# Kernel optimization log

Hardware: AMD Instinct MI355X
Metric: run time of the kernel (lower is better)

## Reference

```python
import jax, jax.numpy as jnp
import numpy as np

N_G, N_D = 100000, 50000
E_GG, E_DG = 1600000, 800000
IN, HID, H, OUT = 128, 128, 8, 2
D = HID // H  # 16


def setup_inputs() -> dict:
    key = jax.random.key(0)
    ks = jax.random.split(key, 14)
    w = lambda k, s: jax.random.normal(k, s, dtype=jnp.float32) * 0.05
    return {
        "x_gene": jax.random.normal(ks[0], (N_G, IN), dtype=jnp.float32),
        "x_disease": jax.random.normal(ks[1], (N_D, IN), dtype=jnp.float32),
        "edge_gg": jax.random.randint(ks[2], (2, E_GG), 0, N_G),   # gene -> gene
        "edge_dg": jax.random.randint(ks[3], (2, E_DG), 0, N_D),   # disease -> gene (dst < N_D <= N_G)
        "proj_gene_w": w(ks[4], (HID, IN)),
        "proj_gene_b": jnp.zeros((HID,), jnp.float32),
        "proj_disease_w": w(ks[5], (HID, IN)),
        "proj_disease_b": jnp.zeros((HID,), jnp.float32),
        "att_src_gg": w(ks[6], (H, D)),
        "att_dst_gg": w(ks[7], (H, D)),
        "att_src_dg": w(ks[8], (H, D)),
        "att_dst_dg": w(ks[9], (H, D)),
        "k_lin_w": w(ks[10], (HID, HID)),
        "k_lin_b": jnp.zeros((HID,), jnp.float32),
        "q": w(ks[11], (HID,)),
        "lin_w": w(ks[12], (OUT, HID)),
        "lin_b": jnp.zeros((OUT,), jnp.float32),
    }


def _edge_type_out(x_src, x_dst, att_src, att_dst, src, dst, num_dst):
    """GAT-style message passing for one edge type. x_*: [N,H,D]."""
    a_s = (x_src * att_src).sum(-1)          # [Ns, H]
    a_d = (x_dst * att_dst).sum(-1)          # [Nd, H]
    a = a_s[src] + a_d[dst]                  # [E, H]
    a = jnp.where(a > 0, a, 0.2 * a)         # leaky_relu(0.2)
    # segment softmax over edges grouped by dst node
    m = jax.ops.segment_max(a, dst, num_segments=num_dst)
    m = jnp.where(jnp.isfinite(m), m, 0.0)
    e = jnp.exp(a - m[dst])
    s = jax.ops.segment_sum(e, dst, num_segments=num_dst)
    alpha = e / (s[dst] + 1e-16)             # [E, H]
    msg = x_src[src] * alpha[:, :, None]     # [E, H, D]
    out = jax.ops.segment_sum(msg, dst, num_segments=num_dst)
    return jax.nn.relu(out.reshape(num_dst, H * D))


def reference(x_gene, x_disease, edge_gg, edge_dg,
              proj_gene_w, proj_gene_b, proj_disease_w, proj_disease_b,
              att_src_gg, att_dst_gg, att_src_dg, att_dst_dg,
              k_lin_w, k_lin_b, q, lin_w, lin_b):
    # per-node-type projection, split into heads
    xg = (x_gene @ proj_gene_w.T + proj_gene_b).reshape(N_G, H, D)
    xd = (x_disease @ proj_disease_w.T + proj_disease_b).reshape(N_D, H, D)

    # node-level attention per edge type (dropout p=0.6 is train-only; eval mode here)
    out_gg = _edge_type_out(xg, xg, att_src_gg, att_dst_gg, edge_gg[0], edge_gg[1], N_G)
    out_dg = _edge_type_out(xd, xg, att_src_dg, att_dst_dg, edge_dg[0], edge_dg[1], N_G)

    # semantic-level attention across metapaths for dst type 'gene'
    outs = jnp.stack([out_gg, out_dg])                  # [2, N_G, HID]
    k = jnp.tanh(outs @ k_lin_w.T + k_lin_b)            # [2, N_G, HID]
    score = (q * k.mean(axis=1)).sum(-1)                # [2]
    attn = jax.nn.softmax(score, axis=0)
    fused = (attn[:, None, None] * outs).sum(0)         # [N_G, HID]

    return fused @ lin_w.T + lin_b                      # [N_G, OUT]
```

## Files before the change

### kernel.cpp

```cpp
#include <hip/hip_runtime.h>
#include <hip/hip_fp16.h>
#include <math.h>

#define NG 100000
#define ND 50000
#define EGG 1600000
#define EDG 800000
#define EALL (EGG + EDG)
#define NALL (NG + NG)
#define HID 128
#define NH 8

#define SHIFT 10
#define BDSTS (1 << SHIFT)
#define NBUK  ((NALL + BDSTS - 1) / BDSTS)
#define BUKCAP 18432
#define S1_CH 3072
#define KM_HALF ((NG + 127) / 128)

#define OFF_OUT_GG 0UL
#define OFF_OUT_DG 6400000UL
#define OFF_XG     12800000UL
#define OFF_XD     19200000UL
#define OFF_ASG    22400000UL
#define OFF_ADG    23200000UL
#define OFF_ADD    24000000UL
#define OFF_ASD    24800000UL
#define OFF_KPART  25200000UL
#define OFF_BCNT   25200256UL
#define ZERO_BASE  OFF_KPART
#define ZERO_CNT   512
#define OFF_ATTN   25200768UL
#define OFF_RP     25200896UL
#define OFF_COL    25400960UL
#define OFF_WTIL   27800960UL
#define OFF_BTIL   27804032UL
#define OFF_WTILD  27804160UL
#define OFF_BTILD  27805184UL

typedef float  f32x4  __attribute__((ext_vector_type(4)));
typedef short  bf16x8 __attribute__((ext_vector_type(8)));
typedef _Float16 f16x8 __attribute__((ext_vector_type(8)));
#define MFMA(a, b, c)  __builtin_amdgcn_mfma_f32_16x16x32_bf16(a, b, c, 0, 0, 0)
#define MFMAH(a, b, c) __builtin_amdgcn_mfma_f32_16x16x32_f16(a, b, c, 0, 0, 0)

#define FMAMIX_LO(ACC, SRC, AL) \
    asm("v_fma_mix_f32 %0, %1, %2, %0 op_sel:[0,0,0] op_sel_hi:[1,0,0]" \
        : "+v"(ACC) : "v"(SRC), "v"(AL))
#define FMAMIX_HI(ACC, SRC, AL) \
    asm("v_fma_mix_f32 %0, %1, %2, %0 op_sel:[1,0,0] op_sel_hi:[1,0,0]" \
        : "+v"(ACC) : "v"(SRC), "v"(AL))

__device__ __forceinline__ unsigned short bf16_rne(float f) {
    unsigned u = __float_as_uint(f);
    u += 0x7FFFu + ((u >> 16) & 1u);
    return (unsigned short)(u >> 16);
}
__device__ __forceinline__ float bf16f(unsigned short h) {
    return __uint_as_float(((unsigned)h) << 16);
}
__device__ __forceinline__ unsigned short f16_bits(float f) {
    __half h = __float2half(f);
    return *(unsigned short*)&h;
}
__device__ __forceinline__ float fast_tanh(float x) {
    x = fminf(fmaxf(x, -15.f), 15.f);
    float t = __expf(2.f * x);
    return (t - 1.f) / (t + 1.f);
}
__device__ __forceinline__ bf16x8 cvt_hi8(f32x4 v0, f32x4 v1) {
    bf16x8 f;
    f[0] = (short)bf16_rne(v0.x); f[1] = (short)bf16_rne(v0.y);
    f[2] = (short)bf16_rne(v0.z); f[3] = (short)bf16_rne(v0.w);
    f[4] = (short)bf16_rne(v1.x); f[5] = (short)bf16_rne(v1.y);
    f[6] = (short)bf16_rne(v1.z); f[7] = (short)bf16_rne(v1.w);
    return f;
}
__device__ __forceinline__ bf16x8 cvt_lo8(f32x4 v0, f32x4 v1, bf16x8 h) {
    bf16x8 f;
    f[0] = (short)bf16_rne(v0.x - bf16f((unsigned short)h[0]));
    f[1] = (short)bf16_rne(v0.y - bf16f((unsigned short)h[1]));
    f[2] = (short)bf16_rne(v0.z - bf16f((unsigned short)h[2]));
    f[3] = (short)bf16_rne(v0.w - bf16f((unsigned short)h[3]));
    f[4] = (short)bf16_rne(v1.x - bf16f((unsigned short)h[4]));
    f[5] = (short)bf16_rne(v1.y - bf16f((unsigned short)h[5]));
    f[6] = (short)bf16_rne(v1.z - bf16f((unsigned short)h[6]));
    f[7] = (short)bf16_rne(v1.w - bf16f((unsigned short)h[7]));
    return f;
}
__device__ __forceinline__ unsigned relu_pk(unsigned u) {
    return u & ~(((u & 0x80008000u) >> 15) * 0xFFFFu);
}
union U4F16 { uint4 u; f16x8 f; };

__global__ void init_zero_k(float* __restrict__ p, int n) {
    int i = blockIdx.x * 256 + threadIdx.x;
    if (i < n) p[i] = 0.f;
}

__device__ __forceinline__ void wtil_body(const float* __restrict__ W,
                                          const float* __restrict__ bias,
                                          const float* __restrict__ a0,
                                          const float* __restrict__ a1,
                                          const float* __restrict__ a2, int natt,
                                          float* __restrict__ wtil, float* __restrict__ btil,
                                          int bid, int nblk) {
    int tot = natt * 8 * 128;
    for (int i = bid * 256 + threadIdx.x; i < tot; i += nblk * 256) {
        int k = i & 127, cc = i >> 7;
        int v = cc >> 3, h = cc & 7;
        const float* av = (v == 0) ? a0 : (v == 1) ? a1 : a2;
        float s = 0.f;
        #pragma unroll
        for (int c = 0; c < 16; c++) s += av[h * 16 + c] * W[(h * 16 + c) * 128 + k];
        wtil[i] = s;
    }
    if (bid == 0 && threadIdx.x < natt * 8) {
        int v = threadIdx.x >> 3, h = threadIdx.x & 7;
        const float* av = (v == 0) ? a0 : (v == 1) ? a1 : a2;
        float s = 0.f;
        #pragma unroll
        for (int c = 0; c < 16; c++) s += av[h * 16 + c] * bias[h * 16 + c];
        btil[threadIdx.x] = s;
    }
}

__global__ void make_wtil_both(const float* __restrict__ Wg, const float* __restrict__ bg,
                               const float* __restrict__ ag0, const float* __restrict__ ag1,
                               const float* __restrict__ ag2,
                               const float* __restrict__ Wd, const float* __restrict__ bd,
                               const float* __restrict__ ad0,
                               float* __restrict__ wtilG, float* __restrict__ btilG,
                               float* __restrict__ wtilD, float* __restrict__ btilD) {
    if (blockIdx.x < 8)
        wtil_body(Wg, bg, ag0, ag1, ag2, 3, wtilG, btilG, blockIdx.x, 8);
    else
        wtil_body(Wd, bd, ad0, ad0, ad0, 1, wtilD, btilD, blockIdx.x - 8, 4);
}

template<int NATT>
__launch_bounds__(256)
__global__ void proj_mfma(const float* __restrict__ x, const float* __restrict__ W,
                          const float* __restrict__ bias,
                          const float* __restrict__ wtil, const float* __restrict__ btil,
                          unsigned short* __restrict__ xbf,
                          float* __restrict__ o0, float* __restrict__ o1,
                          float* __restrict__ o2, int N) {
    constexpr int NTE = (NATT * 8 + 15) / 16;
    constexpr int NT = 8 + NTE;
    __shared__ bf16x8 Bhi[NT * 4 * 64];
    __shared__ bf16x8 Blo[8 * 4 * 64];
    for (int idx = threadIdx.x; idx < 128 * 32; idx += 256) {
        int row = idx >> 5, kq = idx & 31;
        f32x4 v = *(const f32x4*)&W[row * 128 + kq * 4];
        int ct = row >> 4, c = row & 15;
        int k0 = kq * 4;
        int kc = k0 >> 5, q16 = (k0 & 31) >> 3, j2 = (k0 & 7) >> 1;
        int slot = (ct * 4 + kc) * 64 + q16 * 16 + c;
        unsigned short hx = bf16_rne(v.x), hy = bf16_rne(v.y);
        unsigned short hz = bf16_rne(v.z), hw = bf16_rne(v.w);
        unsigned* dh = (unsigned*)&Bhi[slot];
        dh[j2]     = ((unsigned)hy << 16) | hx;
        dh[j2 + 1] = ((unsigned)hw << 16) | hz;
        unsigned* dl = (unsigned*)&Blo[slot];
        dl[j2]     = ((unsigned)bf16_rne(v.y - bf16f(hy)) << 16) | bf16_rne(v.x - bf16f(hx));
        dl[j2 + 1] = ((unsigned)bf16_rne(v.w - bf16f(hw)) << 16) | bf16_rne(v.z - bf16f(hz));
    }
    for (int idx = threadIdx.x; idx < NTE * 16 * 32; idx += 256) {
        int cc = idx >> 5, kq = idx & 31;
        f32x4 v = {0.f, 0.f, 0.f, 0.f};
        if (cc < NATT * 8) v = *(const f32x4*)&wtil[cc * 128 + kq * 4];
        int ct = 8 + (cc >> 4), c = cc & 15;
        int k0 = kq * 4;
        int kc = k0 >> 5, q16 = (k0 & 31) >> 3, j2 = (k0 & 7) >> 1;
        unsigned* dh = (unsigned*)&Bhi[(ct * 4 + kc) * 64 + q16 * 16 + c];
        dh[j2]     = ((unsigned)bf16_rne(v.y) << 16) | bf16_rne(v.x);
        dh[j2 + 1] = ((unsigned)bf16_rne(v.w) << 16) | bf16_rne(v.z);
    }
    __syncthreads();
    int wv = threadIdx.x >> 6, l = threadIdx.x & 63;
    int q = l >> 4, c16 = l & 15;
    int rw = blockIdx.x * 128 + wv * 32;
    int n0 = min(rw + c16, N - 1);
    int n1 = min(rw + 16 + c16, N - 1);
    const float* xr0 = &x[(size_t)n0 * 128 + q * 8];
    const float* xr1 = &x[(size_t)n1 * 128 + q * 8];
    #define LOADX(FH, FL, PTR, OFF) \
        bf16x8 FH, FL; \
        { f32x4 v0_ = *(const f32x4*)((PTR) + (OFF)); \
          f32x4 v1_ = *(const f32x4*)((PTR) + (OFF) + 4); \
          FH = cvt_hi8(v0_, v1_); FL = cvt_lo8(v0_, v1_, FH); }
    LOADX(xh00, xl00, xr0, 0)  LOADX(xh01, xl01, xr0, 32)
    LOADX(xh02, xl02, xr0, 64) LOADX(xh03, xl03, xr0, 96)
    LOADX(xh10, xl10, xr1, 0)  LOADX(xh11, xl11, xr1, 32)
    LOADX(xh12, xl12, xr1, 64) LOADX(xh13, xl13, xr1, 96)
    #undef LOADX
    int r0 = rw + q * 4;
    int r1 = r0 + 16;
    #define CT_MAIN(CT) { \
        bf16x8 bh0 = Bhi[((CT) * 4 + 0) * 64 + l]; \
        bf16x8 bh1 = Bhi[((CT) * 4 + 1) * 64 + l]; \
        bf16x8 bh2 = Bhi[((CT) * 4 + 2) * 64 + l]; \
        bf16x8 bh3 = Bhi[((CT) * 4 + 3) * 64 + l]; \
        bf16x8 bl0 = Blo[((CT) * 4 + 0) * 64 + l]; \
        bf16x8 bl1 = Blo[((CT) * 4 + 1) * 64 + l]; \
        bf16x8 bl2 = Blo[((CT) * 4 + 2) * 64 + l]; \
        bf16x8 bl3 = Blo[((CT) * 4 + 3) * 64 + l]; \
        f32x4 aA = {0,0,0,0}, aB = {0,0,0,0}, aC = {0,0,0,0}, aD = {0,0,0,0}; \
        aA = MFMA(xh00, bh0, aA); aB = MFMA(xh01, bh1, aB); \
        aC = MFMA(xh10, bh0, aC); aD = MFMA(xh11, bh1, aD); \
        aA = MFMA(xl00, bh0, aA); aB = MFMA(xl01, bh1, aB); \
        aC = MFMA(xl10, bh0, aC); aD = MFMA(xl11, bh1, aD); \
        aA = MFMA(xh00, bl0, aA); aB = MFMA(xh01, bl1, aB); \
        aC = MFMA(xh10, bl0, aC); aD = MFMA(xh11, bl1, aD); \
        aA = MFMA(xh02, bh2, aA); aB = MFMA(xh03, bh3, aB); \
        aC = MFMA(xh12, bh2, aC); aD = MFMA(xh13, bh3, aD); \
        aA = MFMA(xl02, bh2, aA); aB = MFMA(xl03, bh3, aB); \
        aC = MFMA(xl12, bh2, aC); aD = MFMA(xl13, bh3, aD); \
        aA = MFMA(xh02, bl2, aA); aB = MFMA(xh03, bl3, aB); \
        aC = MFMA(xh12, bl2, aC); aD = MFMA(xh13, bl3, aD); \
        f32x4 d0 = aA + aB, d1 = aC + aD; \
        float bv = bias[(CT) * 16 + c16]; \
        int col = (CT) * 16 + c16; \
        if (r0 + 0 < N) xbf[(size_t)(r0 + 0) * 128 + col] = f16_bits(d0[0] + bv); \
        if (r0 + 1 < N) xbf[(size_t)(r0 + 1) * 128 + col] = f16_bits(d0[1] + bv); \
        if (r0 + 2 < N) xbf[(size_t)(r0 + 2) * 128 + col] = f16_bits(d0[2] + bv); \
        if (r0 + 3 < N) xbf[(size_t)(r0 + 3) * 128 + col] = f16_bits(d0[3] + bv); \
        if (r1 + 0 < N) xbf[(size_t)(r1 + 0) * 128 + col] = f16_bits(d1[0] + bv); \
        if (r1 + 1 < N) xbf[(size_t)(r1 + 1) * 128 + col] = f16_bits(d1[1] + bv); \
        if (r1 + 2 < N) xbf[(size_t)(r1 + 2) * 128 + col] = f16_bits(d1[2] + bv); \
        if (r1 + 3 < N) xbf[(size_t)(r1 + 3) * 128 + col] = f16_bits(d1[3] + bv); }
    CT_MAIN(0) CT_MAIN(1) CT_MAIN(2) CT_MAIN(3)
    CT_MAIN(4) CT_MAIN(5) CT_MAIN(6) CT_MAIN(7)
    #undef CT_MAIN
    #define CT_ATT(TE) { \
        bf16x8 bh0 = Bhi[((8 + (TE)) * 4 + 0) * 64 + l]; \
        bf16x8 bh1 = Bhi[((8 + (TE)) * 4 + 1) * 64 + l]; \
        bf16x8 bh2 = Bhi[((8 + (TE)) * 4 + 2) * 64 + l]; \
        bf16x8 bh3 = Bhi[((8 + (TE)) * 4 + 3) * 64 + l]; \
        f32x4 aA = {0,0,0,0}, aB = {0,0,0,0}, aC = {0,0,0,0}, aD = {0,0,0,0}; \
        aA = MFMA(xh00, bh0, aA); aB = MFMA(xh01, bh1, aB); \
        aC = MFMA(xh10, bh0, aC); aD = MFMA(xh11, bh1, aD); \
        aA = MFMA(xh02, bh2, aA); aB = MFMA(xh03, bh3, aB); \
        aC = MFMA(xh12, bh2, aC); aD = MFMA(xh13, bh3, aD); \
        f32x4 d0 = aA + aB, d1 = aC + aD; \
        int cc = (TE) * 16 + c16; \
        if (cc < NATT * 8) { \
            float bt = btil[cc]; \
            int v = cc >> 3, h = cc & 7; \
            float* op = (v == 0) ? o0 : ((v == 1) ? o1 : o2); \
            if (r0 + 0 < N) op[(r0 + 0) * 8 + h] = d0[0] + bt; \
            if (r0 + 1 < N) op[(r0 + 1) * 8 + h] = d0[1] + bt; \
            if (r0 + 2 < N) op[(r0 + 2) * 8 + h] = d0[2] + bt; \
            if (r0 + 3 < N) op[(r0 + 3) * 8 + h] = d0[3] + bt; \
            if (r1 + 0 < N) op[(r1 + 0) * 8 + h] = d1[0] + bt; \
            if (r1 + 1 < N) op[(r1 + 1) * 8 + h] = d1[1] + bt; \
            if (r1 + 2 < N) op[(r1 + 2) * 8 + h] = d1[2] + bt; \
            if (r1 + 3 < N) op[(r1 + 3) * 8 + h] = d1[3] + bt; } }
    CT_ATT(0)
    if constexpr (NTE > 1) { CT_ATT(1) }
    #undef CT_ATT
}

__launch_bounds__(256)
__global__ void fused_scatter(const int* __restrict__ gg_src, const int* __restrict__ gg_dst,
                              const int* __restrict__ dg_src, const int* __restrict__ dg_dst,
                              int* __restrict__ bcnt, unsigned int* __restrict__ colPacked) {
    __shared__ int cnt[256], scanE[256], gbase[256], cursor[256];
    __shared__ int ss[256];
    __shared__ unsigned int sorted[S1_CH];
    __shared__ unsigned char bof[S1_CH];
    int t = threadIdx.x;
    cnt[t] = 0;
    __syncthreads();
    int base = blockIdx.x * S1_CH;
    for (int k = 0; k < S1_CH; k += 256) {
        int e = base + k + t;
        if (e < EALL) {
            int dn = (e < EGG) ? gg_dst[e] : (NG + dg_dst[e - EGG]);
            atomicAdd(&cnt[dn >> SHIFT], 1);
        }
    }
    __syncthreads();
    int v = cnt[t];
    ss[t] = v;
    __syncthreads();
    for (int off = 1; off < 256; off <<= 1) {
        int y = (t >= off) ? ss[t - off] : 0;
        __syncthreads();
        ss[t] += y;
        __syncthreads();
    }
    scanE[t] = ss[t] - v;
    cursor[t] = ss[t] - v;
    if (t < NBUK && v > 0) gbase[t] = atomicAdd(&bcnt[t], v);
    __syncthreads();
    for (int k = 0; k < S1_CH; k += 256) {
        int e = base + k + t;
        if (e < EALL) {
            int s, dn;
            if (e < EGG) { s = gg_src[e]; dn = gg_dst[e]; }
            else         { s = dg_src[e - EGG]; dn = NG + dg_dst[e - EGG]; }
            int b = dn >> SHIFT;
            int slot = atomicAdd(&cursor[b], 1);
            sorted[slot] = ((unsigned int)s << SHIFT) | (unsigned int)(dn & (BDSTS - 1));
            bof[slot] = (unsigned char)b;
        }
    }
    __syncthreads();
    int total = ss[255];
    for (int f = t; f < total; f += 256) {
        int b = bof[f];
        colPacked[(size_t)b * BUKCAP + gbase[b] + (f - scanE[b])] = sorted[f];
    }
}

__launch_bounds__(256)
__global__ void bucket_build(const unsigned int* __restrict__ colPacked,
                             const int* __restrict__ bcnt,
                             int* __restrict__ rp, int* __restrict__ col) {
    __shared__ int lcur[BDSTS];
    __shared__ int tsum[256];
    __shared__ int bscan[256];
    int b = blockIdx.x;
    int t = threadIdx.x;
    bscan[t] = (t < NBUK) ? bcnt[t] : 0;
    __syncthreads();
    for (int off = 1; off < 256; off <<= 1) {
        int y = (t >= off) ? bscan[t - off] : 0;
        __syncthreads();
        bscan[t] += y;
        __syncthreads();
    }
    int gb = (b > 0) ? bscan[b - 1] : 0;
    int d0 = b << SHIFT;
    int nd = min(BDSTS, NALL - d0);
    int cnt = bcnt[b];
    const unsigned int* pk = colPacked + (size_t)b * BUKCAP;
    for (int i = t; i < BDSTS; i += 256) lcur[i] = 0;
    __syncthreads();
    for (int i = t; i < cnt; i += 256)
        atomicAdd(&lcur[pk[i] & (BDSTS - 1)], 1);
    __syncthreads();
    int h0 = lcur[t * 4 + 0], h1 = lcur[t * 4 + 1], h2 = lcur[t * 4 + 2], h3 = lcur[t * 4 + 3];
    int tot = h0 + h1 + h2 + h3;
    tsum[t] = tot;
    __syncthreads();
    for (int off = 1; off < 256; off <<= 1) {
        int y = (t >= off) ? tsum[t - off] : 0;
        __syncthreads();
        tsum[t] += y;
        __syncthreads();
    }
    int pp = tsum[t] - tot + gb;
    __syncthreads();
    #define EMIT(J, HJ) { int idx = t * 4 + (J); \
        if (idx < nd) rp[d0 + idx] = pp; \
        lcur[idx] = pp; pp += (HJ); }
    EMIT(0, h0) EMIT(1, h1) EMIT(2, h2) EMIT(3, h3)
    #undef EMIT
    if (b == NBUK - 1 && t == 0) rp[NALL] = EALL;
    __syncthreads();
    for (int i = t; i < cnt; i += 256) {
        unsigned int p = pk[i];
        int pos = atomicAdd(&lcur[p & (BDSTS - 1)], 1);
        col[pos] = (int)(p >> SHIFT);
    }
}

__launch_bounds__(256)
__global__ void gat_gather_all(const int* __restrict__ rp, const int* __restrict__ col,
                               const float* __restrict__ as_gg, const float* __restrict__ ad_gg,
                               const unsigned short* __restrict__ xg_h,
                               const float* __restrict__ as_dg, const float* __restrict__ ad_dg,
                               const unsigned short* __restrict__ xd_h,
                               unsigned short* __restrict__ out_gg,
                               unsigned short* __restrict__ out_dg) {
    int wid = (blockIdx.x * 256 + threadIdx.x) >> 6;
    int l = threadIdx.x & 63;
    if (wid >= NALL) return;
    int isdg = wid >= NG;
    int d = isdg ? wid - NG : wid;
    const float* a_s = isdg ? as_dg : as_gg;
    const float* a_d = isdg ? ad_dg : ad_gg;
    const unsigned short* xbf = isdg ? xd_h : xg_h;
    unsigned short* outh = (isdg ? out_dg : out_gg);

    int base = rp[wid];
    int deg = rp[wid + 1] - base;

    int hl = l & 7;
    int g  = l >> 3;
    float adl = a_d[d * 8 + hl];
    int q = l >> 4;
    int cq = l & 15;
    int hq = cq >> 1;
    uint32_t colbyte = (uint32_t)cq << 4;
    float a0 = 0.f, a1 = 0.f, a2 = 0.f, a3 = 0.f, a4 = 0.f, a5 = 0.f, a6 = 0.f, a7 = 0.f;
    float sacc = 0.f;
    for (int c0 = 0; c0 < deg; c0 += 64) {
        int myi = c0 + l;
        int colreg = (myi < deg) ? col[base + myi] : 0;
        int lim = min(deg - c0, 64);
        for (int j8 = 0; j8 < lim; j8 += 8) {
            float ex;
            {
                int s = __shfl(colreg, j8 + g);
                float a = a_s[s * 8 + hl] + adl;
                a = a > 0.f ? a : 0.2f * a;
                ex = __expf(a);
            }
            int jlim = min(lim - j8, 8);
            #pragma unroll
            for (int sub = 0; sub < 8; sub += 4) {
                int jrel = sub + q;
                int s = __shfl(colreg, j8 + jrel);
                float al = __shfl(ex, (jrel << 3) + hq);
                al = (jrel < jlim) ? al : 0.f;
                sacc += al;
                const uint4 rv = *(const uint4*)((const char*)xbf +
                                    (((size_t)(uint32_t)s << 8) + colbyte));
                FMAMIX_LO(a0, rv.x, al); FMAMIX_HI(a1, rv.x, al);
                FMAMIX_LO(a2, rv.y, al); FMAMIX_HI(a3, rv.y, al);
                FMAMIX_LO(a4, rv.z, al); FMAMIX_HI(a5, rv.z, al);
                FMAMIX_LO(a6, rv.w, al); FMAMIX_HI(a7, rv.w, al);
            }
        }
    }
    sacc += __shfl_xor(sacc, 16); sacc += __shfl_xor(sacc, 32);
    a0 += __shfl_xor(a0, 16); a0 += __shfl_xor(a0, 32);
    a1 += __shfl_xor(a1, 16); a1 += __shfl_xor(a1, 32);
    a2 += __shfl_xor(a2, 16); a2 += __shfl_xor(a2, 32);
    a3 += __shfl_xor(a3, 16); a3 += __shfl_xor(a3, 32);
    a4 += __shfl_xor(a4, 16); a4 += __shfl_xor(a4, 32);
    a5 += __shfl_xor(a5, 16); a5 += __shfl_xor(a5, 32);
    a6 += __shfl_xor(a6, 16); a6 += __shfl_xor(a6, 32);
    a7 += __shfl_xor(a7, 16); a7 += __shfl_xor(a7, 32);
    if (q == 0) {
        float rsc = 1.f / (sacc + 1e-16f);
        a0 *= rsc; a1 *= rsc; a2 *= rsc; a3 *= rsc;
        a4 *= rsc; a5 *= rsc; a6 *= rsc; a7 *= rsc;
        __half2 h01 = __floats2half2_rn(a0, a1);
        __half2 h23 = __floats2half2_rn(a2, a3);
        __half2 h45 = __floats2half2_rn(a4, a5);
        __half2 h67 = __floats2half2_rn(a6, a7);
        uint4 o;
        o.x = *(unsigned*)&h01; o.y = *(unsigned*)&h23;
        o.z = *(unsigned*)&h45; o.w = *(unsigned*)&h67;
        *(uint4*)((char*)outh + (size_t)d * 256 + cq * 16) = o;
    }
}

__launch_bounds__(256)
__global__ void kmean_mfma(const unsigned short* __restrict__ srcA,
                           const unsigned short* __restrict__ srcB,
                           const float* __restrict__ W, const float* __restrict__ bias,
                           float* __restrict__ kp) {
    __shared__ f16x8 Bs[8 * 4 * 64];
    for (int idx = threadIdx.x; idx < 128 * 32; idx += 256) {
        int row = idx >> 5, kq = idx & 31;
        f32x4 v = *(const f32x4*)&W[row * 128 + kq * 4];
        int ct = row >> 4, c = row & 15;
        int k0 = kq * 4;
        int kc = k0 >> 5, q16 = (k0 & 31) >> 3, j2 = (k0 & 7) >> 1;
        unsigned* dst = (unsigned*)&Bs[(ct * 4 + kc) * 64 + q16 * 16 + c];
        dst[j2]     = ((unsigned)f16_bits(v.y) << 16) | f16_bits(v.x);
        dst[j2 + 1] = ((unsigned)f16_bits(v.w) << 16) | f16_bits(v.z);
    }
    __syncthreads();
    int half = blockIdx.x >= KM_HALF;
    const unsigned short* src = half ? srcB : srcA;
    float* kpp = half ? (kp + 128) : kp;
    int rb = (half ? blockIdx.x - KM_HALF : blockIdx.x) * 128;
    int wv = threadIdx.x >> 6, l = threadIdx.x & 63;
    int q = l >> 4, c16 = l & 15;
    int rw = rb + wv * 32;
    const char* xr0 = (const char*)src + (size_t)(rw + c16) * 256 + q * 16;
    const char* xr1 = xr0 + 16 * 256;
    #define LOADA(F, PTR, OFF) f16x8 F; { \
        U4F16 u_; u_.u = *(const uint4*)((PTR) + (OFF)); \
        u_.u.x = relu_pk(u_.u.x); u_.u.y = relu_pk(u_.u.y); \
        u_.u.z = relu_pk(u_.u.z); u_.u.w = relu_pk(u_.u.w); \
        F = u_.f; }
    LOADA(f00, xr0, 0) LOADA(f01, xr0, 64) LOADA(f02, xr0, 128) LOADA(f03, xr0, 192)
    LOADA(f10, xr1, 0) LOADA(f11, xr1, 64) LOADA(f12, xr1, 128) LOADA(f13, xr1, 192)
    #undef LOADA
    float bv0 = bias[c16],      bv1 = bias[16 + c16], bv2 = bias[32 + c16], bv3 = bias[48 + c16];
    float bv4 = bias[64 + c16], bv5 = bias[80 + c16], bv6 = bias[96 + c16], bv7 = bias[112 + c16];
    int row0 = rw + q * 4;
    int row1 = row0 + 16;
    float cs0 = 0.f, cs1 = 0.f, cs2 = 0.f, cs3 = 0.f, cs4 = 0.f, cs5 = 0.f, cs6 = 0.f, cs7 = 0.f;
    #define CT_STEP(CT, CS, BV) { \
        f16x8 b0 = Bs[((CT) * 4 + 0) * 64 + l]; \
        f16x8 b1 = Bs[((CT) * 4 + 1) * 64 + l]; \
        f16x8 b2 = Bs[((CT) * 4 + 2) * 64 + l]; \
        f16x8 b3 = Bs[((CT) * 4 + 3) * 64 + l]; \
        f32x4 aA = {0,0,0,0}, aB = {0,0,0,0}, aC = {0,0,0,0}, aD = {0,0,0,0}; \
        aA = MFMAH(f00, b0, aA); aB = MFMAH(f01, b1, aB); \
        aA = MFMAH(f02, b2, aA); aB = MFMAH(f03, b3, aB); \
        aC = MFMAH(f10, b0, aC); aD = MFMAH(f11, b1, aD); \
        aC = MFMAH(f12, b2, aC); aD = MFMAH(f13, b3, aD); \
        f32x4 d0 = aA + aB, d1 = aC + aD; \
        float s = 0.f; \
        if (row0 + 0 < NG) s += fast_tanh(d0[0] + (BV)); \
        if (row0 + 1 < NG) s += fast_tanh(d0[1] + (BV)); \
        if (row0 + 2 < NG) s += fast_tanh(d0[2] + (BV)); \
        if (row0 + 3 < NG) s += fast_tanh(d0[3] + (BV)); \
        if (row1 + 0 < NG) s += fast_tanh(d1[0] + (BV)); \
        if (row1 + 1 < NG) s += fast_tanh(d1[1] + (BV)); \
        if (row1 + 2 < NG) s += fast_tanh(d1[2] + (BV)); \
        if (row1 + 3 < NG) s += fast_tanh(d1[3] + (BV)); \
        CS += s; }
    CT_STEP(0, cs0, bv0) CT_STEP(1, cs1, bv1) CT_STEP(2, cs2, bv2) CT_STEP(3, cs3, bv3)
    CT_STEP(4, cs4, bv4) CT_STEP(5, cs5, bv5) CT_STEP(6, cs6, bv6) CT_STEP(7, cs7, bv7)
    #undef CT_STEP
    __syncthreads();
    float* red = (float*)Bs;
    #define REDUCE_CT(CT, CS) { \
        float v = (CS); \
        v += __shfl_xor(v, 16); v += __shfl_xor(v, 32); \
        if (l < 16) red[wv * 128 + (CT) * 16 + l] = v; }
    REDUCE_CT(0, cs0) REDUCE_CT(1, cs1) REDUCE_CT(2, cs2) REDUCE_CT(3, cs3)
    REDUCE_CT(4, cs4) REDUCE_CT(5, cs5) REDUCE_CT(6, cs6) REDUCE_CT(7, cs7)
    #undef REDUCE_CT
    __syncthreads();
    if (threadIdx.x < 128) {
        float s = red[threadIdx.x] + red[128 + threadIdx.x]
                + red[256 + threadIdx.x] + red[384 + threadIdx.x];
        atomicAdd(&kpp[threadIdx.x], s);
    }
}

__global__ void score_attn(const float* __restrict__ kpart, const float* __restrict__ q,
                           float* __restrict__ attn) {
    __shared__ float r0[128], r1[128];
    int t = threadIdx.x;
    r0[t] = q[t] * kpart[t];
    r1[t] = q[t] * kpart[128 + t];
    __syncthreads();
    for (int s = 64; s > 0; s >>= 1) {
        if (t < s) { r0[t] += r0[t + s]; r1[t] += r1[t + s]; }
        __syncthreads();
    }
    if (t == 0) {
        float s0 = r0[0] / (float)NG, s1 = r1[0] / (float)NG;
        float mx = fmaxf(s0, s1);
        float e0 = expf(s0 - mx), e1 = expf(s1 - mx);
        attn[0] = e0 / (e0 + e1);
        attn[1] = e1 / (e0 + e1);
    }
}

__launch_bounds__(256)
__global__ void final_lin(const unsigned short* __restrict__ gg,
                          const unsigned short* __restrict__ dgb,
                          const float* __restrict__ attn, const float* __restrict__ lin_w,
                          const float* __restrict__ lin_b, float* __restrict__ outp) {
    int wid = (blockIdx.x * 256 + threadIdx.x) >> 6;
    int l = threadIdx.x & 63;
    if (wid >= NG) return;
    float a0 = attn[0], a1 = attn[1];
    unsigned gu = *(const unsigned*)((const char*)gg + (size_t)wid * 256 + l * 4);
    unsigned du = *(const unsigned*)((const char*)dgb + (size_t)wid * 256 + l * 4);
    float2 gv = __half22float2(*(const __half2*)&gu);
    float2 dv = __half22float2(*(const __half2*)&du);
    float fx = a0 * fmaxf(gv.x, 0.f) + a1 * fmaxf(dv.x, 0.f);
    float fy = a0 * fmaxf(gv.y, 0.f) + a1 * fmaxf(dv.y, 0.f);
    float2 w0 = *(const float2*)&lin_w[l * 2];
    float2 w1 = *(const float2*)&lin_w[128 + l * 2];
    float p0 = fx * w0.x + fy * w0.y;
    float p1 = fx * w1.x + fy * w1.y;
    for (int off = 32; off > 0; off >>= 1) {
        p0 += __shfl_down(p0, off);
        p1 += __shfl_down(p1, off);
    }
    if (l == 0) {
        float2 o;
        o.x = p0 + lin_b[0];
        o.y = p1 + lin_b[1];
        *(float2*)&outp[wid * 2] = o;
    }
}

extern "C" void kernel_launch(void* const* d_in, const int* in_sizes, int n_in,
                              void* d_out, int out_size, void* d_ws, size_t ws_size,
                              hipStream_t stream) {
    const float* x_gene    = (const float*)d_in[0];
    const float* x_disease = (const float*)d_in[1];
    const int*   edge_gg   = (const int*)d_in[2];
    const int*   edge_dg   = (const int*)d_in[3];
    const float* pg_w      = (const float*)d_in[4];
    const float* pg_b      = (const float*)d_in[5];
    const float* pd_w      = (const float*)d_in[6];
    const float* pd_b      = (const float*)d_in[7];
    const float* att_src_gg= (const float*)d_in[8];
    const float* att_dst_gg= (const float*)d_in[9];
    const float* att_src_dg= (const float*)d_in[10];
    const float* att_dst_dg= (const float*)d_in[11];
    const float* k_lin_w   = (const float*)d_in[12];
    const float* k_lin_b   = (const float*)d_in[13];
    const float* q         = (const float*)d_in[14];
    const float* lin_w     = (const float*)d_in[15];
    const float* lin_b     = (const float*)d_in[16];
    float* out = (float*)d_out;
    float* ws  = (float*)d_ws;

    unsigned short* out_gg = (unsigned short*)(ws + OFF_OUT_GG);
    unsigned short* out_dg = (unsigned short*)(ws + OFF_OUT_DG);
    unsigned int* colPacked = (unsigned int*)(ws + OFF_OUT_GG);
    unsigned short* xg_h = (unsigned short*)(ws + OFF_XG);
    unsigned short* xd_h = (unsigned short*)(ws + OFF_XD);
    float* a_src_gg = ws + OFF_ASG;
    float* a_dst_gg = ws + OFF_ADG;
    float* a_dst_dg = ws + OFF_ADD;
    float* a_src_dg = ws + OFF_ASD;
    float* kpart  = ws + OFF_KPART;
    float* attn   = ws + OFF_ATTN;
    float* wtilG  = ws + OFF_WTIL;
    float* btilG  = ws + OFF_BTIL;
    float* wtilD  = ws + OFF_WTILD;
    float* btilD  = ws + OFF_BTILD;
    int* bcnt  = (int*)(ws + OFF_BCNT);
    int* rp    = (int*)(ws + OFF_RP);
    int* col   = (int*)(ws + OFF_COL);

    const int* gg_src = edge_gg;
    const int* gg_dst = edge_gg + EGG;
    const int* dg_src = edge_dg;
    const int* dg_dst = edge_dg + EDG;

    hipLaunchKernelGGL(init_zero_k, dim3(2), dim3(256), 0, stream, ws + ZERO_BASE, ZERO_CNT);
    hipLaunchKernelGGL(make_wtil_both, dim3(12), dim3(256), 0, stream,
                       pg_w, pg_b, att_src_gg, att_dst_gg, att_dst_dg,
                       pd_w, pd_b, att_src_dg, wtilG, btilG, wtilD, btilD);
    hipLaunchKernelGGL((proj_mfma<3>), dim3((NG + 127) / 128), dim3(256), 0, stream,
                       x_gene, pg_w, pg_b, wtilG, btilG, xg_h,
                       a_src_gg, a_dst_gg, a_dst_dg, NG);
    hipLaunchKernelGGL((proj_mfma<1>), dim3((ND + 127) / 128), dim3(256), 0, stream,
                       x_disease, pd_w, pd_b, wtilD, btilD, xd_h,
                       a_src_dg, (float*)nullptr, (float*)nullptr, ND);
    hipLaunchKernelGGL(fused_scatter, dim3((EALL + S1_CH - 1) / S1_CH), dim3(256), 0, stream,
                       gg_src, gg_dst, dg_src, dg_dst, bcnt, colPacked);
    hipLaunchKernelGGL(bucket_build, dim3(NBUK), dim3(256), 0, stream,
                       colPacked, bcnt, rp, col);
    hipLaunchKernelGGL(gat_gather_all, dim3((NALL + 3) / 4), dim3(256), 0, stream,
                       rp, col, a_src_gg, a_dst_gg, xg_h, a_src_dg, a_dst_dg, xd_h,
                       out_gg, out_dg);
    hipLaunchKernelGGL(kmean_mfma, dim3(KM_HALF * 2), dim3(256), 0, stream,
                       out_gg, out_dg, k_lin_w, k_lin_b, kpart);
    hipLaunchKernelGGL(score_attn, dim3(1), dim3(128), 0, stream, kpart, q, attn);
    hipLaunchKernelGGL(final_lin, dim3((NG + 3) / 4), dim3(256), 0, stream,
                       out_gg, out_dg, attn, lin_w, lin_b, out);
}
```

Baseline: 327.1 us.

## Merge projection kernels and fold final linear projection into gather

Drops the separate wtil kernel. Each projection block now computes its attention-folded weights and biases in shared memory, and the gene and disease projections run as one launch. The final linear layer is applied per metapath inside the gather kernel, which writes 2-wide partial outputs, so the last kernel only mixes them with the attention weights instead of re-reading both 128-wide fp16 outputs. The gather does a little more work per node, and every projection block repeats the wtil computation.

```diff
diff --git a/kernel.cpp b/kernel.cpp
--- a/kernel.cpp
+++ b/kernel.cpp
@@ -17,6 +17,8 @@
 #define BUKCAP 18432
 #define S1_CH 3072
 #define KM_HALF ((NG + 127) / 128)
+#define GBLK ((NG + 127) / 128)
+#define DBLK ((ND + 127) / 128)
 
 #define OFF_OUT_GG 0UL
 #define OFF_OUT_DG 6400000UL
@@ -33,10 +35,8 @@
 #define OFF_ATTN   25200768UL
 #define OFF_RP     25200896UL
 #define OFF_COL    25400960UL
-#define OFF_WTIL   27800960UL
-#define OFF_BTIL   27804032UL
-#define OFF_WTILD  27804160UL
-#define OFF_BTILD  27805184UL
+#define OFF_PGG    27801088UL
+#define OFF_PDG    28001088UL
 
 typedef float  f32x4  __attribute__((ext_vector_type(4)));
 typedef short  bf16x8 __attribute__((ext_vector_type(8)));
@@ -98,58 +98,35 @@
     if (i < n) p[i] = 0.f;
 }
 
-__device__ __forceinline__ void wtil_body(const float* __restrict__ W,
-                                          const float* __restrict__ bias,
-                                          const float* __restrict__ a0,
-                                          const float* __restrict__ a1,
-                                          const float* __restrict__ a2, int natt,
-                                          float* __restrict__ wtil, float* __restrict__ btil,
-                                          int bid, int nblk) {
-    int tot = natt * 8 * 128;
-    for (int i = bid * 256 + threadIdx.x; i < tot; i += nblk * 256) {
-        int k = i & 127, cc = i >> 7;
-        int v = cc >> 3, h = cc & 7;
-        const float* av = (v == 0) ? a0 : (v == 1) ? a1 : a2;
-        float s = 0.f;
-        #pragma unroll
-        for (int c = 0; c < 16; c++) s += av[h * 16 + c] * W[(h * 16 + c) * 128 + k];
-        wtil[i] = s;
-    }
-    if (bid == 0 && threadIdx.x < natt * 8) {
-        int v = threadIdx.x >> 3, h = threadIdx.x & 7;
-        const float* av = (v == 0) ? a0 : (v == 1) ? a1 : a2;
-        float s = 0.f;
-        #pragma unroll
-        for (int c = 0; c < 16; c++) s += av[h * 16 + c] * bias[h * 16 + c];
-        btil[threadIdx.x] = s;
-    }
-}
-
-__global__ void make_wtil_both(const float* __restrict__ Wg, const float* __restrict__ bg,
-                               const float* __restrict__ ag0, const float* __restrict__ ag1,
-                               const float* __restrict__ ag2,
-                               const float* __restrict__ Wd, const float* __restrict__ bd,
-                               const float* __restrict__ ad0,
-                               float* __restrict__ wtilG, float* __restrict__ btilG,
-                               float* __restrict__ wtilD, float* __restrict__ btilD) {
-    if (blockIdx.x < 8)
-        wtil_body(Wg, bg, ag0, ag1, ag2, 3, wtilG, btilG, blockIdx.x, 8);
-    else
-        wtil_body(Wd, bd, ad0, ad0, ad0, 1, wtilD, btilD, blockIdx.x - 8, 4);
-}
-
-template<int NATT>
 __launch_bounds__(256)
-__global__ void proj_mfma(const float* __restrict__ x, const float* __restrict__ W,
-                          const float* __restrict__ bias,
-                          const float* __restrict__ wtil, const float* __restrict__ btil,
-                          unsigned short* __restrict__ xbf,
-                          float* __restrict__ o0, float* __restrict__ o1,
-                          float* __restrict__ o2, int N) {
-    constexpr int NTE = (NATT * 8 + 15) / 16;
-    constexpr int NT = 8 + NTE;
-    __shared__ bf16x8 Bhi[NT * 4 * 64];
+__global__ void proj_both(const float* __restrict__ xg, const float* __restrict__ Wg,
+                          const float* __restrict__ bg,
+                          const float* __restrict__ ag0, const float* __restrict__ ag1,
+                          const float* __restrict__ ag2,
+                          unsigned short* __restrict__ xgh,
+                          float* __restrict__ og0, float* __restrict__ og1,
+                          float* __restrict__ og2,
+                          const float* __restrict__ xd, const float* __restrict__ Wd,
+                          const float* __restrict__ bd, const float* __restrict__ ad0,
+                          unsigned short* __restrict__ xdh, float* __restrict__ od0) {
+    __shared__ bf16x8 Bhi[10 * 4 * 64];
     __shared__ bf16x8 Blo[8 * 4 * 64];
+    __shared__ float btilS[32];
+    int gene = blockIdx.x < GBLK;
+    const float* x    = gene ? xg : xd;
+    const float* W    = gene ? Wg : Wd;
+    const float* bias = gene ? bg : bd;
+    const float* a0v  = gene ? ag0 : ad0;
+    const float* a1v  = gene ? ag1 : ad0;
+    const float* a2v  = gene ? ag2 : ad0;
+    unsigned short* xbf = gene ? xgh : xdh;
+    float* o0 = gene ? og0 : od0;
+    float* o1 = og1;
+    float* o2 = og2;
+    int ccmax = gene ? 24 : 8;
+    int N = gene ? NG : ND;
+    int bid = gene ? blockIdx.x : blockIdx.x - GBLK;
+
     for (int idx = threadIdx.x; idx < 128 * 32; idx += 256) {
         int row = idx >> 5, kq = idx & 31;
         f32x4 v = *(const f32x4*)&W[row * 128 + kq * 4];
@@ -166,10 +143,19 @@
         dl[j2]     = ((unsigned)bf16_rne(v.y - bf16f(hy)) << 16) | bf16_rne(v.x - bf16f(hx));
         dl[j2 + 1] = ((unsigned)bf16_rne(v.w - bf16f(hw)) << 16) | bf16_rne(v.z - bf16f(hz));
     }
-    for (int idx = threadIdx.x; idx < NTE * 16 * 32; idx += 256) {
+    for (int idx = threadIdx.x; idx < 2 * 16 * 32; idx += 256) {
         int cc = idx >> 5, kq = idx & 31;
         f32x4 v = {0.f, 0.f, 0.f, 0.f};
-        if (cc < NATT * 8) v = *(const f32x4*)&wtil[cc * 128 + kq * 4];
+        if (cc < ccmax) {
+            int vv = cc >> 3, h = cc & 7;
+            const float* av = (vv == 0) ? a0v : (vv == 1) ? a1v : a2v;
+            #pragma unroll
+            for (int c = 0; c < 16; c++) {
+                float a = av[h * 16 + c];
+                f32x4 w = *(const f32x4*)&W[(h * 16 + c) * 128 + kq * 4];
+                v.x += a * w.x; v.y += a * w.y; v.z += a * w.z; v.w += a * w.w;
+            }
+        }
         int ct = 8 + (cc >> 4), c = cc & 15;
         int k0 = kq * 4;
         int kc = k0 >> 5, q16 = (k0 & 31) >> 3, j2 = (k0 & 7) >> 1;
@@ -177,10 +163,20 @@
         dh[j2]     = ((unsigned)bf16_rne(v.y) << 16) | bf16_rne(v.x);
         dh[j2 + 1] = ((unsigned)bf16_rne(v.w) << 16) | bf16_rne(v.z);
     }
+    if (threadIdx.x < 32) {
+        float s = 0.f;
+        if (threadIdx.x < ccmax) {
+            int vv = threadIdx.x >> 3, h = threadIdx.x & 7;
+            const float* av = (vv == 0) ? a0v : (vv == 1) ? a1v : a2v;
+            #pragma unroll
+            for (int c = 0; c < 16; c++) s += av[h * 16 + c] * bias[h * 16 + c];
+        }
+        btilS[threadIdx.x] = s;
+    }
     __syncthreads();
     int wv = threadIdx.x >> 6, l = threadIdx.x & 63;
     int q = l >> 4, c16 = l & 15;
-    int rw = blockIdx.x * 128 + wv * 32;
+    int rw = bid * 128 + wv * 32;
     int n0 = min(rw + c16, N - 1);
     int n1 = min(rw + 16 + c16, N - 1);
     const float* xr0 = &x[(size_t)n0 * 128 + q * 8];
@@ -245,10 +241,10 @@
         aC = MFMA(xh12, bh2, aC); aD = MFMA(xh13, bh3, aD); \
         f32x4 d0 = aA + aB, d1 = aC + aD; \
         int cc = (TE) * 16 + c16; \
-        if (cc < NATT * 8) { \
-            float bt = btil[cc]; \
-            int v = cc >> 3, h = cc & 7; \
-            float* op = (v == 0) ? o0 : ((v == 1) ? o1 : o2); \
+        if (cc < ccmax) { \
+            float bt = btilS[cc]; \
+            int vv = cc >> 3, h = cc & 7; \
+            float* op = (vv == 0) ? o0 : ((vv == 1) ? o1 : o2); \
             if (r0 + 0 < N) op[(r0 + 0) * 8 + h] = d0[0] + bt; \
             if (r0 + 1 < N) op[(r0 + 1) * 8 + h] = d0[1] + bt; \
             if (r0 + 2 < N) op[(r0 + 2) * 8 + h] = d0[2] + bt; \
@@ -258,7 +254,7 @@
             if (r1 + 2 < N) op[(r1 + 2) * 8 + h] = d1[2] + bt; \
             if (r1 + 3 < N) op[(r1 + 3) * 8 + h] = d1[3] + bt; } }
     CT_ATT(0)
-    if constexpr (NTE > 1) { CT_ATT(1) }
+    if (ccmax > 16) { CT_ATT(1) }
     #undef CT_ATT
 }
 
@@ -375,7 +371,9 @@
                                const float* __restrict__ as_dg, const float* __restrict__ ad_dg,
                                const unsigned short* __restrict__ xd_h,
                                unsigned short* __restrict__ out_gg,
-                               unsigned short* __restrict__ out_dg) {
+                               unsigned short* __restrict__ out_dg,
+                               const float* __restrict__ lin_w,
+                               float* __restrict__ pgg, float* __restrict__ pdg) {
     int wid = (blockIdx.x * 256 + threadIdx.x) >> 6;
     int l = threadIdx.x & 63;
     if (wid >= NALL) return;
@@ -448,6 +446,25 @@
         o.x = *(unsigned*)&h01; o.y = *(unsigned*)&h23;
         o.z = *(unsigned*)&h45; o.w = *(unsigned*)&h67;
         *(uint4*)((char*)outh + (size_t)d * 256 + cq * 16) = o;
+        float r0 = fmaxf(a0, 0.f), r1 = fmaxf(a1, 0.f), r2 = fmaxf(a2, 0.f), r3 = fmaxf(a3, 0.f);
+        float r4 = fmaxf(a4, 0.f), r5 = fmaxf(a5, 0.f), r6 = fmaxf(a6, 0.f), r7 = fmaxf(a7, 0.f);
+        f32x4 w0a = *(const f32x4*)&lin_w[cq * 8];
+        f32x4 w0b = *(const f32x4*)&lin_w[cq * 8 + 4];
+        f32x4 w1a = *(const f32x4*)&lin_w[128 + cq * 8];
+        f32x4 w1b = *(const f32x4*)&lin_w[128 + cq * 8 + 4];
+        float p0 = r0 * w0a.x + r1 * w0a.y + r2 * w0a.z + r3 * w0a.w
+                 + r4 * w0b.x + r5 * w0b.y + r6 * w0b.z + r7 * w0b.w;
+        float p1 = r0 * w1a.x + r1 * w1a.y + r2 * w1a.z + r3 * w1a.w
+                 + r4 * w1b.x + r5 * w1b.y + r6 * w1b.z + r7 * w1b.w;
+        p0 += __shfl_xor(p0, 1); p1 += __shfl_xor(p1, 1);
+        p0 += __shfl_xor(p0, 2); p1 += __shfl_xor(p1, 2);
+        p0 += __shfl_xor(p0, 4); p1 += __shfl_xor(p1, 4);
+        p0 += __shfl_xor(p0, 8); p1 += __shfl_xor(p1, 8);
+        if (l == 0) {
+            float* pp = isdg ? pdg : pgg;
+            float2 pv; pv.x = p0; pv.y = p1;
+            *(float2*)&pp[d * 2] = pv;
+        }
     }
 }
 
@@ -551,35 +568,18 @@
     }
 }
 
-__launch_bounds__(256)
-__global__ void final_lin(const unsigned short* __restrict__ gg,
-                          const unsigned short* __restrict__ dgb,
-                          const float* __restrict__ attn, const float* __restrict__ lin_w,
-                          const float* __restrict__ lin_b, float* __restrict__ outp) {
-    int wid = (blockIdx.x * 256 + threadIdx.x) >> 6;
-    int l = threadIdx.x & 63;
-    if (wid >= NG) return;
+__global__ void final_combine(const float* __restrict__ pgg, const float* __restrict__ pdg,
+                              const float* __restrict__ attn, const float* __restrict__ lin_b,
+                              float* __restrict__ outp) {
+    int n = blockIdx.x * 256 + threadIdx.x;
+    if (n >= NG) return;
     float a0 = attn[0], a1 = attn[1];
-    unsigned gu = *(const unsigned*)((const char*)gg + (size_t)wid * 256 + l * 4);
-    unsigned du = *(const unsigned*)((const char*)dgb + (size_t)wid * 256 + l * 4);
-    float2 gv = __half22float2(*(const __half2*)&gu);
-    float2 dv = __half22float2(*(const __half2*)&du);
-    float fx = a0 * fmaxf(gv.x, 0.f) + a1 * fmaxf(dv.x, 0.f);
-    float fy = a0 * fmaxf(gv.y, 0.f) + a1 * fmaxf(dv.y, 0.f);
-    float2 w0 = *(const float2*)&lin_w[l * 2];
-    float2 w1 = *(const float2*)&lin_w[128 + l * 2];
-    float p0 = fx * w0.x + fy * w0.y;
-    float p1 = fx * w1.x + fy * w1.y;
-    for (int off = 32; off > 0; off >>= 1) {
-        p0 += __shfl_down(p0, off);
-        p1 += __shfl_down(p1, off);
-    }
-    if (l == 0) {
-        float2 o;
-        o.x = p0 + lin_b[0];
-        o.y = p1 + lin_b[1];
-        *(float2*)&outp[wid * 2] = o;
-    }
+    float2 g = *(const float2*)&pgg[n * 2];
+    float2 dd = *(const float2*)&pdg[n * 2];
+    float2 o;
+    o.x = a0 * g.x + a1 * dd.x + lin_b[0];
+    o.y = a0 * g.y + a1 * dd.y + lin_b[1];
+    *(float2*)&outp[n * 2] = o;
 }
 
 extern "C" void kernel_launch(void* const* d_in, const int* in_sizes, int n_in,
@@ -616,10 +616,8 @@
     float* a_src_dg = ws + OFF_ASD;
     float* kpart  = ws + OFF_KPART;
     float* attn   = ws + OFF_ATTN;
-    float* wtilG  = ws + OFF_WTIL;
-    float* btilG  = ws + OFF_BTIL;
-    float* wtilD  = ws + OFF_WTILD;
-    float* btilD  = ws + OFF_BTILD;
+    float* pgg    = ws + OFF_PGG;
+    float* pdg    = ws + OFF_PDG;
     int* bcnt  = (int*)(ws + OFF_BCNT);
     int* rp    = (int*)(ws + OFF_RP);
     int* col   = (int*)(ws + OFF_COL);
@@ -630,25 +628,20 @@
     const int* dg_dst = edge_dg + EDG;
 
     hipLaunchKernelGGL(init_zero_k, dim3(2), dim3(256), 0, stream, ws + ZERO_BASE, ZERO_CNT);
-    hipLaunchKernelGGL(make_wtil_both, dim3(12), dim3(256), 0, stream,
-                       pg_w, pg_b, att_src_gg, att_dst_gg, att_dst_dg,
-                       pd_w, pd_b, att_src_dg, wtilG, btilG, wtilD, btilD);
-    hipLaunchKernelGGL((proj_mfma<3>), dim3((NG + 127) / 128), dim3(256), 0, stream,
-                       x_gene, pg_w, pg_b, wtilG, btilG, xg_h,
-                       a_src_gg, a_dst_gg, a_dst_dg, NG);
-    hipLaunchKernelGGL((proj_mfma<1>), dim3((ND + 127) / 128), dim3(256), 0, stream,
-                       x_disease, pd_w, pd_b, wtilD, btilD, xd_h,
-                       a_src_dg, (float*)nullptr, (float*)nullptr, ND);
+    hipLaunchKernelGGL(proj_both, dim3(GBLK + DBLK), dim3(256), 0, stream,
+                       x_gene, pg_w, pg_b, att_src_gg, att_dst_gg, att_dst_dg,
+                       xg_h, a_src_gg, a_dst_gg, a_dst_dg,
+                       x_disease, pd_w, pd_b, att_src_dg, xd_h, a_src_dg);
     hipLaunchKernelGGL(fused_scatter, dim3((EALL + S1_CH - 1) / S1_CH), dim3(256), 0, stream,
                        gg_src, gg_dst, dg_src, dg_dst, bcnt, colPacked);
     hipLaunchKernelGGL(bucket_build, dim3(NBUK), dim3(256), 0, stream,
                        colPacked, bcnt, rp, col);
     hipLaunchKernelGGL(gat_gather_all, dim3((NALL + 3) / 4), dim3(256), 0, stream,
                        rp, col, a_src_gg, a_dst_gg, xg_h, a_src_dg, a_dst_dg, xd_h,
-                       out_gg, out_dg);
+                       out_gg, out_dg, lin_w, pgg, pdg);
     hipLaunchKernelGGL(kmean_mfma, dim3(KM_HALF * 2), dim3(256), 0, stream,
                        out_gg, out_dg, k_lin_w, k_lin_b, kpart);
     hipLaunchKernelGGL(score_attn, dim3(1), dim3(128), 0, stream, kpart, q, attn);
-    hipLaunchKernelGGL(final_lin, dim3((NG + 3) / 4), dim3(256), 0, stream,
-                       out_gg, out_dg, attn, lin_w, lin_b, out);
-}
+    hipLaunchKernelGGL(final_combine, dim3((NG + 255) / 256), dim3(256), 0, stream,
+                       pgg, pdg, attn, lin_b, out);
+}
```

New measurement: 312.7 us. 4.4% less time.
